# Performance work log

Hardware: AMD Instinct MI355X
Metric: run time of the kernel (lower is better)

Reference implementation:

```python
import jax, jax.numpy as jnp
import numpy as np

NQ = 4            # num_qubits
DIM = 2 ** NQ     # 16-dim complex state

def _rx(theta):
    c = jnp.cos(theta / 2.0); s = jnp.sin(theta / 2.0)
    return jnp.array([[c, -1j * s], [-1j * s, c]], dtype=jnp.complex64)

def _ry(theta):
    c = jnp.cos(theta / 2.0); s = jnp.sin(theta / 2.0)
    return jnp.array([[c, -s], [s, c]], dtype=jnp.complex64)

def _apply_1q(state, q, U):
    # state: [B, 16] complex; apply 2x2 unitary U on qubit q (qubit 0 = MSB)
    B = state.shape[0]
    st = state.reshape((B,) + (2,) * NQ)
    st = jnp.moveaxis(st, 1 + q, -1)
    st = st @ U.T
    st = jnp.moveaxis(st, -1, 1 + q)
    return st.reshape(B, DIM)

def _apply_cnot(state, c, t):
    # flip target qubit t where control qubit c == 1
    B = state.shape[0]
    st = state.reshape((B,) + (2,) * NQ)
    st = jnp.moveaxis(st, (1 + c, 1 + t), (-2, -1))
    st = jnp.stack([st[..., 0, :], st[..., 1, ::-1]], axis=-2)
    st = jnp.moveaxis(st, (-2, -1), (1 + c, 1 + t))
    return st.reshape(B, DIM)

def _circuit(state):
    rx1, ry1 = _rx(0.1), _ry(0.2)
    rx2, ry2 = _rx(0.3), _ry(0.4)
    for q in range(NQ):
        state = _apply_1q(state, q, rx1)
        state = _apply_1q(state, q, ry1)
    for q in range(NQ - 1):
        state = _apply_cnot(state, q, q + 1)
    for q in range(NQ):
        state = _apply_1q(state, q, rx2)
        state = _apply_1q(state, q, ry2)
    return state

def setup_inputs() -> dict:
    key = jax.random.key(0)
    ks = jax.random.split(key, 9)
    B = 65536
    return {
        'x':   jax.random.normal(ks[0], (B, 784), dtype=jnp.float32),
        'We1': jax.random.normal(ks[1], (784, 256), dtype=jnp.float32) * 0.05,
        'be1': jnp.zeros((256,), dtype=jnp.float32),
        'We2': jax.random.normal(ks[2], (256, 32), dtype=jnp.float32) * 0.05,
        'be2': jnp.zeros((32,), dtype=jnp.float32),
        'W1':  jax.random.normal(ks[3], (32, 128), dtype=jnp.float32) * 0.05,
        'b1':  jnp.zeros((128,), dtype=jnp.float32),
        'W2':  jax.random.normal(ks[4], (128, 10), dtype=jnp.float32) * 0.05,
        'b2':  jnp.zeros((10,), dtype=jnp.float32),
    }

def reference(x, We1, be1, We2, be2, W1, b1, W2, b2):
    # encoder: Linear(784,256) -> ReLU -> Linear(256,32) -> Tanh
    h = jax.nn.relu(x @ We1 + be1)
    enc = jnp.tanh(h @ We2 + be2)               # [B, 32]
    psi = (enc[:, :DIM] + 1j * enc[:, DIM:]).astype(jnp.complex64)
    norm = jnp.sqrt(jnp.sum(jnp.abs(psi) ** 2, axis=1, keepdims=True))
    psi = psi / norm
    psi = _circuit(psi)                          # [B, 16] complex
    feat = jnp.concatenate([psi.real, psi.imag], axis=1)  # [B, 32]
    # classifier: Linear(32,128) -> ReLU -> (Dropout=identity in eval) -> Linear(128,10)
    out = jax.nn.relu(feat @ W1 + b1) @ W2 + b2
    return out
```

## Files before the change

### kernel.cpp

```cpp
#include <hip/hip_runtime.h>
#include <stdint.h>

#define DEVINL __device__ __forceinline__

typedef short bf16x8 __attribute__((ext_vector_type(8)));
typedef float f32x4  __attribute__((ext_vector_type(4)));

DEVINL uint16_t f2bf(float f) {
    uint32_t u = __builtin_bit_cast(uint32_t, f);
    uint32_t r = u + 0x7fffu + ((u >> 16) & 1u);
    return (uint16_t)(r >> 16);
}

DEVINL f32x4 mfma16x16x32(bf16x8 a, bf16x8 b, f32x4 c) {
    return __builtin_amdgcn_mfma_f32_16x16x32_bf16(a, b, c, 0, 0, 0);
}

DEVINL void async_load16(const void* g, void* l) {
    __builtin_amdgcn_global_load_lds(
        (const __attribute__((address_space(1))) void*)g,
        (__attribute__((address_space(3))) void*)l, 16, 0, 0);
}

#define WS_WE1T 0
#define WS_WE2T 409600
#define WS_W1T  425984
#define WS_W2T  434176

__global__ __launch_bounds__(256) void prep_weights(
    const float* __restrict__ We1, const float* __restrict__ We2,
    const float* __restrict__ W1,  const float* __restrict__ W2,
    uint16_t* __restrict__ We1T, uint16_t* __restrict__ We2T,
    uint16_t* __restrict__ W1T,  uint16_t* __restrict__ W2T) {
    int tid = blockIdx.x * 256 + threadIdx.x;
    if (tid < 256 * 800) {
        int n = tid / 800, k = tid % 800;
        We1T[tid] = (k < 784) ? f2bf(We1[k * 256 + n]) : (uint16_t)0;
        return;
    }
    int t2 = tid - 256 * 800;
    if (t2 < 32 * 256) {
        int n = t2 / 256, k = t2 % 256;
        We2T[t2] = f2bf(We2[k * 32 + n]);
        return;
    }
    int t3 = t2 - 32 * 256;
    if (t3 < 128 * 32) {
        int n = t3 / 32, k = t3 % 32;
        W1T[t3] = f2bf(W1[k * 128 + n]);
        return;
    }
    int t4 = t3 - 128 * 32;
    if (t4 < 16 * 128) {
        int n = t4 / 128, k = t4 % 128;
        W2T[t4] = (n < 10) ? f2bf(W2[k * 10 + n]) : (uint16_t)0;
        return;
    }
}

DEVINL void apply_rx(float* sr, float* si, int bit, float c, float s) {
    #pragma unroll
    for (int i = 0; i < 16; i++) {
        if (!(i & bit)) {
            int j = i | bit;
            float r0 = sr[i], i0 = si[i], r1 = sr[j], i1 = si[j];
            sr[i] = c * r0 + s * i1;  si[i] = c * i0 - s * r1;
            sr[j] = c * r1 + s * i0;  si[j] = c * i1 - s * r0;
        }
    }
}
DEVINL void apply_ry(float* sr, float* si, int bit, float c, float s) {
    #pragma unroll
    for (int i = 0; i < 16; i++) {
        if (!(i & bit)) {
            int j = i | bit;
            float r0 = sr[i], i0 = si[i], r1 = sr[j], i1 = si[j];
            sr[i] = c * r0 - s * r1;  si[i] = c * i0 - s * i1;
            sr[j] = s * r0 + c * r1;  si[j] = s * i0 + c * i1;
        }
    }
}
DEVINL void apply_cnot(float* sr, float* si, int cb, int tb) {
    #pragma unroll
    for (int i = 0; i < 16; i++) {
        if ((i & cb) && !(i & tb)) {
            int j = i | tb;
            float tr = sr[i]; sr[i] = sr[j]; sr[j] = tr;
            float ti = si[i]; si[i] = si[j]; si[j] = ti;
        }
    }
}
DEVINL void circuit(float* sr, float* si) {
    const float C1 = 0.99875026039496628f, S1 = 0.04997916927067833f;
    const float C2 = 0.99500416527802582f, S2 = 0.09983341664682815f;
    const float C3 = 0.98877107793604227f, S3 = 0.14943813247359922f;
    const float C4 = 0.98006657784124163f, S4 = 0.19866933079506122f;
    #pragma unroll
    for (int q = 0; q < 4; q++) {
        int bit = 8 >> q;
        apply_rx(sr, si, bit, C1, S1);
        apply_ry(sr, si, bit, C2, S2);
    }
    apply_cnot(sr, si, 8, 4);
    apply_cnot(sr, si, 4, 2);
    apply_cnot(sr, si, 2, 1);
    #pragma unroll
    for (int q = 0; q < 4; q++) {
        int bit = 8 >> q;
        apply_rx(sr, si, bit, C3, S3);
        apply_ry(sr, si, bit, C4, S4);
    }
}

__global__ __launch_bounds__(256, 4) void fused_kernel(
    const float* __restrict__ x, const uint16_t* __restrict__ We1T,
    const float* __restrict__ be1,
    const uint16_t* __restrict__ We2T, const float* __restrict__ be2,
    const uint16_t* __restrict__ W1T, const float* __restrict__ b1,
    const uint16_t* __restrict__ W2T, const float* __restrict__ b2,
    float* __restrict__ out) {
    __shared__ __align__(16) char smem[34816];
    uint16_t* Als   = (uint16_t*)smem;
    uint16_t* Bls   = (uint16_t*)(smem + 4096);
    uint16_t* Htile = (uint16_t*)smem;
    float*    encls  = (float*)smem;
    uint16_t* featls = (uint16_t*)(smem + 8448);
    uint16_t* a1ls   = (uint16_t*)(smem + 13568);

    const int t = threadIdx.x;
    const int rowbase = blockIdx.x * 64;
    const int w  = t >> 6;
    const int l  = t & 63;
    const int lm = l & 15;
    const int lq = l >> 4;

    f32x4 acc[4][4] = {};

    const int ar = t >> 2;
    const int aq = t & 3;
    const float* xrow = x + (size_t)(rowbase + ar) * 784;

    float4 va0 = *(const float4*)(xrow + aq * 8);
    float4 va1 = *(const float4*)(xrow + aq * 8 + 4);

    for (int k0 = 0; k0 < 800; k0 += 32) {
        __syncthreads();

        #pragma unroll
        for (int j = 0; j < 4; j++) {
            int g = j * 256 + t;
            async_load16(We1T + (size_t)(g >> 2) * 800 + (g & 3) * 8 + k0, &Bls[8 * g]);
        }
        union { uint4 u4; uint16_t us[8]; } pk;
        pk.us[0] = f2bf(va0.x); pk.us[1] = f2bf(va0.y);
        pk.us[2] = f2bf(va0.z); pk.us[3] = f2bf(va0.w);
        pk.us[4] = f2bf(va1.x); pk.us[5] = f2bf(va1.y);
        pk.us[6] = f2bf(va1.z); pk.us[7] = f2bf(va1.w);
        *(uint4*)&Als[8 * t] = pk.u4;
        {
            int kn = k0 + 32;
            if (kn < 800) {
                int c = kn + aq * 8;
                if (c < 784) {
                    va0 = *(const float4*)(xrow + c);
                    va1 = *(const float4*)(xrow + c + 4);
                } else {
                    va0 = make_float4(0.f, 0.f, 0.f, 0.f);
                    va1 = make_float4(0.f, 0.f, 0.f, 0.f);
                }
            }
        }
        __syncthreads();

        bf16x8 afr[4], bfr[4];
        #pragma unroll
        for (int mi = 0; mi < 4; mi++)
            afr[mi] = *(const bf16x8*)&Als[(mi * 16 + lm) * 32 + lq * 8];
        #pragma unroll
        for (int ni = 0; ni < 4; ni++)
            bfr[ni] = *(const bf16x8*)&Bls[(w * 64 + ni * 16 + lm) * 32 + lq * 8];
        #pragma unroll
        for (int mi = 0; mi < 4; mi++)
            #pragma unroll
            for (int ni = 0; ni < 4; ni++)
                acc[mi][ni] = mfma16x16x32(afr[mi], bfr[ni], acc[mi][ni]);
    }

    __syncthreads();

    #pragma unroll
    for (int ni = 0; ni < 4; ni++) {
        int n = w * 64 + ni * 16 + lm;
        float bias = be1[n];
        #pragma unroll
        for (int mi = 0; mi < 4; mi++) {
            #pragma unroll
            for (int i = 0; i < 4; i++) {
                int r = mi * 16 + lq * 4 + i;
                float v = acc[mi][ni][i] + bias;
                v = v > 0.f ? v : 0.f;
                Htile[r * 272 + n] = f2bf(v);
            }
        }
    }
    __syncthreads();

    f32x4 acc2[2] = {};
    #pragma unroll
    for (int k0 = 0; k0 < 256; k0 += 32) {
        bf16x8 af = *(const bf16x8*)&Htile[(w * 16 + lm) * 272 + k0 + lq * 8];
        #pragma unroll
        for (int ni = 0; ni < 2; ni++) {
            bf16x8 bf = *(const bf16x8*)&We2T[(ni * 16 + lm) * 256 + k0 + lq * 8];
            acc2[ni] = mfma16x16x32(af, bf, acc2[ni]);
        }
    }
    __syncthreads();

    #pragma unroll
    for (int ni = 0; ni < 2; ni++) {
        int col = ni * 16 + lm;
        float bias = be2[col];
        #pragma unroll
        for (int i = 0; i < 4; i++) {
            int r = w * 16 + lq * 4 + i;
            encls[r * 33 + col] = tanhf(acc2[ni][i] + bias);
        }
    }
    __syncthreads();

    if (t < 64) {
        float e[32];
        #pragma unroll
        for (int j = 0; j < 32; j++) e[j] = encls[t * 33 + j];
        float s = 0.f;
        #pragma unroll
        for (int j = 0; j < 32; j++) s += e[j] * e[j];
        float inv = 1.0f / sqrtf(s);
        float sr[16], si[16];
        #pragma unroll
        for (int i = 0; i < 16; i++) { sr[i] = e[i] * inv; si[i] = e[16 + i] * inv; }
        circuit(sr, si);
        #pragma unroll
        for (int i = 0; i < 16; i++) {
            featls[t * 40 + i]      = f2bf(sr[i]);
            featls[t * 40 + 16 + i] = f2bf(si[i]);
        }
    }
    __syncthreads();

    f32x4 acc3[8] = {};
    {
        bf16x8 af = *(const bf16x8*)&featls[(w * 16 + lm) * 40 + lq * 8];
        #pragma unroll
        for (int ni = 0; ni < 8; ni++) {
            bf16x8 bf = *(const bf16x8*)&W1T[(ni * 16 + lm) * 32 + lq * 8];
            acc3[ni] = mfma16x16x32(af, bf, acc3[ni]);
        }
    }
    #pragma unroll
    for (int ni = 0; ni < 8; ni++) {
        int col = ni * 16 + lm;
        float bias = b1[col];
        #pragma unroll
        for (int i = 0; i < 4; i++) {
            int r = w * 16 + lq * 4 + i;
            float v = acc3[ni][i] + bias;
            v = v > 0.f ? v : 0.f;
            a1ls[r * 136 + col] = f2bf(v);
        }
    }

    f32x4 acc4 = {};
    #pragma unroll
    for (int k0 = 0; k0 < 128; k0 += 32) {
        bf16x8 af = *(const bf16x8*)&a1ls[(w * 16 + lm) * 136 + k0 + lq * 8];
        bf16x8 bf = *(const bf16x8*)&W2T[lm * 128 + k0 + lq * 8];
        acc4 = mfma16x16x32(af, bf, acc4);
    }
    if (lm < 10) {
        float bias = b2[lm];
        #pragma unroll
        for (int i = 0; i < 4; i++) {
            int r = rowbase + w * 16 + lq * 4 + i;
            out[(size_t)r * 10 + lm] = acc4[i] + bias;
        }
    }
}

extern "C" void kernel_launch(void* const* d_in, const int* in_sizes, int n_in,
                              void* d_out, int out_size, void* d_ws, size_t ws_size,
                              hipStream_t stream) {
    const float* x   = (const float*)d_in[0];
    const float* We1 = (const float*)d_in[1];
    const float* be1 = (const float*)d_in[2];
    const float* We2 = (const float*)d_in[3];
    const float* be2 = (const float*)d_in[4];
    const float* W1  = (const float*)d_in[5];
    const float* b1  = (const float*)d_in[6];
    const float* W2  = (const float*)d_in[7];
    const float* b2  = (const float*)d_in[8];
    float* out = (float*)d_out;

    char* ws = (char*)d_ws;
    uint16_t* We1T = (uint16_t*)(ws + WS_WE1T);
    uint16_t* We2T = (uint16_t*)(ws + WS_WE2T);
    uint16_t* W1T  = (uint16_t*)(ws + WS_W1T);
    uint16_t* W2T  = (uint16_t*)(ws + WS_W2T);

    hipLaunchKernelGGL(prep_weights, dim3(856), dim3(256), 0, stream,
                       We1, We2, W1, W2, We1T, We2T, W1T, W2T);
    hipLaunchKernelGGL(fused_kernel, dim3(1024), dim3(256), 0, stream,
                       x, We1T, be1, We2T, be2, W1T, b1, W2T, b2, out);
}
```

Measured before the change: 322.8 us.

## Double K-tile to 64 and XOR-swizzle LDS layout for first GEMM

The first GEMM's K step grows from 32 to 64, with We1T padded to 832 columns, so each block runs half as many barrier-separated iterations and issues two MFMA rounds per tile. The A and B tiles in LDS use an XOR swizzle on 16-byte chunks to cut bank conflicts on fragment reads. Shared memory grows to 40 KB, each thread holds more prefetch registers, and the padding adds 48 zero K columns of wasted MFMA work.

```diff
diff --git a/kernel.cpp b/kernel.cpp
--- a/kernel.cpp
+++ b/kernel.cpp
@@ -23,9 +23,9 @@
 }
 
 #define WS_WE1T 0
-#define WS_WE2T 409600
-#define WS_W1T  425984
-#define WS_W2T  434176
+#define WS_WE2T 425984
+#define WS_W1T  442368
+#define WS_W2T  450560
 
 __global__ __launch_bounds__(256) void prep_weights(
     const float* __restrict__ We1, const float* __restrict__ We2,
@@ -33,12 +33,12 @@
     uint16_t* __restrict__ We1T, uint16_t* __restrict__ We2T,
     uint16_t* __restrict__ W1T,  uint16_t* __restrict__ W2T) {
     int tid = blockIdx.x * 256 + threadIdx.x;
-    if (tid < 256 * 800) {
-        int n = tid / 800, k = tid % 800;
+    if (tid < 256 * 832) {
+        int n = tid / 832, k = tid % 832;
         We1T[tid] = (k < 784) ? f2bf(We1[k * 256 + n]) : (uint16_t)0;
         return;
     }
-    int t2 = tid - 256 * 800;
+    int t2 = tid - 256 * 832;
     if (t2 < 32 * 256) {
         int n = t2 / 256, k = t2 % 256;
         We2T[t2] = f2bf(We2[k * 32 + n]);
@@ -119,9 +119,9 @@
     const uint16_t* __restrict__ W1T, const float* __restrict__ b1,
     const uint16_t* __restrict__ W2T, const float* __restrict__ b2,
     float* __restrict__ out) {
-    __shared__ __align__(16) char smem[34816];
+    __shared__ __align__(16) char smem[40960];
     uint16_t* Als   = (uint16_t*)smem;
-    uint16_t* Bls   = (uint16_t*)(smem + 4096);
+    uint16_t* Bls   = (uint16_t*)(smem + 8192);
     uint16_t* Htile = (uint16_t*)smem;
     float*    encls  = (float*)smem;
     uint16_t* featls = (uint16_t*)(smem + 8448);
@@ -137,53 +137,76 @@
     f32x4 acc[4][4] = {};
 
     const int ar = t >> 2;
-    const int aq = t & 3;
+    const int ac = (t & 3) * 16;
     const float* xrow = x + (size_t)(rowbase + ar) * 784;
-
-    float4 va0 = *(const float4*)(xrow + aq * 8);
-    float4 va1 = *(const float4*)(xrow + aq * 8 + 4);
-
-    for (int k0 = 0; k0 < 800; k0 += 32) {
+    const int aswz = ar & 7;
+    const int ach0 = ((t & 3) * 2)     ^ aswz;
+    const int ach1 = ((t & 3) * 2 + 1) ^ aswz;
+
+    float4 va[4];
+    #pragma unroll
+    for (int j = 0; j < 4; j++) {
+        int c = ac + j * 4;
+        va[j] = (c < 784) ? *(const float4*)(xrow + c) : make_float4(0.f, 0.f, 0.f, 0.f);
+    }
+
+    for (int k0 = 0; k0 < 832; k0 += 64) {
         __syncthreads();
 
         #pragma unroll
-        for (int j = 0; j < 4; j++) {
-            int g = j * 256 + t;
-            async_load16(We1T + (size_t)(g >> 2) * 800 + (g & 3) * 8 + k0, &Bls[8 * g]);
-        }
-        union { uint4 u4; uint16_t us[8]; } pk;
-        pk.us[0] = f2bf(va0.x); pk.us[1] = f2bf(va0.y);
-        pk.us[2] = f2bf(va0.z); pk.us[3] = f2bf(va0.w);
-        pk.us[4] = f2bf(va1.x); pk.us[5] = f2bf(va1.y);
-        pk.us[6] = f2bf(va1.z); pk.us[7] = f2bf(va1.w);
-        *(uint4*)&Als[8 * t] = pk.u4;
+        for (int j = 0; j < 8; j++) {
+            int g  = j * 256 + t;
+            int br = g >> 3;
+            int bc = ((g & 7) ^ (br & 7)) * 8;
+            async_load16(We1T + (size_t)br * 832 + k0 + bc, &Bls[8 * g]);
+        }
+        union { uint4 u4; uint16_t us[8]; } p0, p1;
+        p0.us[0] = f2bf(va[0].x); p0.us[1] = f2bf(va[0].y);
+        p0.us[2] = f2bf(va[0].z); p0.us[3] = f2bf(va[0].w);
+        p0.us[4] = f2bf(va[1].x); p0.us[5] = f2bf(va[1].y);
+        p0.us[6] = f2bf(va[1].z); p0.us[7] = f2bf(va[1].w);
+        p1.us[0] = f2bf(va[2].x); p1.us[1] = f2bf(va[2].y);
+        p1.us[2] = f2bf(va[2].z); p1.us[3] = f2bf(va[2].w);
+        p1.us[4] = f2bf(va[3].x); p1.us[5] = f2bf(va[3].y);
+        p1.us[6] = f2bf(va[3].z); p1.us[7] = f2bf(va[3].w);
+        *(uint4*)&Als[ar * 64 + ach0 * 8] = p0.u4;
+        *(uint4*)&Als[ar * 64 + ach1 * 8] = p1.u4;
+
+        __syncthreads();
+
         {
-            int kn = k0 + 32;
-            if (kn < 800) {
-                int c = kn + aq * 8;
-                if (c < 784) {
-                    va0 = *(const float4*)(xrow + c);
-                    va1 = *(const float4*)(xrow + c + 4);
-                } else {
-                    va0 = make_float4(0.f, 0.f, 0.f, 0.f);
-                    va1 = make_float4(0.f, 0.f, 0.f, 0.f);
+            int kn = k0 + 64;
+            if (kn < 832) {
+                #pragma unroll
+                for (int j = 0; j < 4; j++) {
+                    int c = kn + ac + j * 4;
+                    va[j] = (c < 784) ? *(const float4*)(xrow + c)
+                                      : make_float4(0.f, 0.f, 0.f, 0.f);
                 }
             }
         }
-        __syncthreads();
-
-        bf16x8 afr[4], bfr[4];
-        #pragma unroll
-        for (int mi = 0; mi < 4; mi++)
-            afr[mi] = *(const bf16x8*)&Als[(mi * 16 + lm) * 32 + lq * 8];
-        #pragma unroll
-        for (int ni = 0; ni < 4; ni++)
-            bfr[ni] = *(const bf16x8*)&Bls[(w * 64 + ni * 16 + lm) * 32 + lq * 8];
-        #pragma unroll
-        for (int mi = 0; mi < 4; mi++)
+
+        #pragma unroll
+        for (int kk = 0; kk < 2; kk++) {
+            bf16x8 afr[4], bfr[4];
             #pragma unroll
-            for (int ni = 0; ni < 4; ni++)
-                acc[mi][ni] = mfma16x16x32(afr[mi], bfr[ni], acc[mi][ni]);
+            for (int mi = 0; mi < 4; mi++) {
+                int row = mi * 16 + lm;
+                int ch  = (kk * 4 + lq) ^ (lm & 7);
+                afr[mi] = *(const bf16x8*)&Als[row * 64 + ch * 8];
+            }
+            #pragma unroll
+            for (int ni = 0; ni < 4; ni++) {
+                int row = w * 64 + ni * 16 + lm;
+                int ch  = (kk * 4 + lq) ^ (lm & 7);
+                bfr[ni] = *(const bf16x8*)&Bls[row * 64 + ch * 8];
+            }
+            #pragma unroll
+            for (int mi = 0; mi < 4; mi++)
+                #pragma unroll
+                for (int ni = 0; ni < 4; ni++)
+                    acc[mi][ni] = mfma16x16x32(afr[mi], bfr[ni], acc[mi][ni]);
+        }
     }
 
     __syncthreads();
@@ -308,7 +331,7 @@
     uint16_t* W1T  = (uint16_t*)(ws + WS_W1T);
     uint16_t* W2T  = (uint16_t*)(ws + WS_W2T);
 
-    hipLaunchKernelGGL(prep_weights, dim3(856), dim3(256), 0, stream,
+    hipLaunchKernelGGL(prep_weights, dim3(888), dim3(256), 0, stream,
                        We1, We2, W1, W2, We1T, We2T, W1T, W2T);
     hipLaunchKernelGGL(fused_kernel, dim3(1024), dim3(256), 0, stream,
                        x, We1T, be1, We2T, be2, W1T, b1, W2T, b2, out);
```

New measurement: 333.9 us. 3.4% more time.
